# Kernel optimization log

Measured on AMD Instinct MI355X. Metric: run time of the kernel, lower is better.

The kernel has to match this reference:

```python
import jax, jax.numpy as jnp
import numpy as np
import math

B, N, D, H = 2, 2048, 512, 8
DH = D // H
HID = int(D * 16 / 3)  # 2730, SwiGLU hidden; chunks into 1365+1365
EPS = 1e-5


def _get_slopes(n):
    # n=8 is a power of two
    start = 2.0 ** (-2.0 ** (-(math.log2(n) - 3)))
    return np.array([start * (start ** i) for i in range(n)], dtype=np.float32)

_SLOPES = jnp.asarray(_get_slopes(H))  # [H]


def _ln(x, w, b):
    m = jnp.mean(x, axis=-1, keepdims=True)
    v = jnp.mean((x - m) ** 2, axis=-1, keepdims=True)
    return (x - m) * jax.lax.rsqrt(v + EPS) * w + b


def setup_inputs() -> dict:
    key = jax.random.key(0)
    ks = jax.random.split(key, 20)
    p = lambda k, s: jax.random.normal(k, s, jnp.float32) * 0.02
    return {
        "x": jax.random.normal(ks[0], (B, N, D), jnp.float32),
        "coords": jax.random.uniform(ks[1], (B, N, 2), jnp.float32) * 100.0,
        "q_w": p(ks[2], (D, D)), "q_b": jnp.zeros((D,), jnp.float32),
        "k_w": p(ks[3], (D, D)), "k_b": jnp.zeros((D,), jnp.float32),
        "v_w": p(ks[4], (D, D)), "v_b": jnp.zeros((D,), jnp.float32),
        "o_w": p(ks[5], (D, D)), "o_b": jnp.zeros((D,), jnp.float32),
        "gamma1": jnp.ones((D,), jnp.float32),
        "ln1_w": jnp.ones((D,), jnp.float32), "ln1_b": jnp.zeros((D,), jnp.float32),
        "fc1_w": p(ks[6], (HID, D)), "fc1_b": jnp.zeros((HID,), jnp.float32),
        "fc2_w": p(ks[7], (D, HID // 2)), "fc2_b": jnp.zeros((D,), jnp.float32),
        "gamma2": jnp.ones((D,), jnp.float32),
        "ln2_w": jnp.ones((D,), jnp.float32), "ln2_b": jnp.zeros((D,), jnp.float32),
    }


def reference(x, coords, q_w, q_b, k_w, k_b, v_w, v_b, o_w, o_b, gamma1,
              ln1_w, ln1_b, fc1_w, fc1_b, fc2_w, fc2_b, gamma2, ln2_w, ln2_b):
    # ---- residual1: distance-ALiBi attention (eval mode: x + gamma1*attn(norm(x)))
    xn = _ln(x, ln1_w, ln1_b)
    q = (xn @ q_w.T + q_b).reshape(B, N, H, DH).transpose(0, 2, 1, 3)  # [b,h,n,dh]
    k = (xn @ k_w.T + k_b).reshape(B, N, H, DH).transpose(0, 2, 1, 3)
    v = (xn @ v_w.T + v_b).reshape(B, N, H, DH).transpose(0, 2, 1, 3)
    # pairwise Euclidean distance of tile coords -> [b,n,n]
    diff = coords[:, :, None, :] - coords[:, None, :, :]
    dist = jnp.sqrt(jnp.sum(diff * diff, axis=-1))
    attn_bias = -_SLOPES[None, :, None, None] * dist[:, None, :, :]  # [b,h,n,n]
    scale = 1.0 / math.sqrt(DH)
    scores = jnp.einsum('bhqd,bhkd->bhqk', q, k) * scale + attn_bias
    attn = jax.nn.softmax(scores, axis=-1)
    ctx = jnp.einsum('bhqk,bhkd->bhqd', attn, v)
    ctx = ctx.transpose(0, 2, 1, 3).reshape(B, N, D)
    attn_out = ctx @ o_w.T + o_b
    x = x + gamma1 * attn_out
    # ---- residual2: SwiGLU-style MLP (eval mode: x + gamma2*mlp(norm(x)))
    xn2 = _ln(x, ln2_w, ln2_b)
    hpre = xn2 @ fc1_w.T + fc1_b  # [b,n,HID]
    h1, h2 = jnp.split(hpre, 2, axis=-1)
    mlp_out = (jax.nn.silu(h1) * h2) @ fc2_w.T + fc2_b
    return x + gamma2 * mlp_out
```

## Files before the change

kernel.cpp:

```cpp
#include <hip/hip_runtime.h>
#include <math.h>

#define Bdim  2
#define Nseq  2048
#define Dmod  512
#define Hn    8
#define DHd   64
#define HID   2730
#define HHALF 1365
#define HC    1408
#define NPACK 2816
#define ROWS  4096
#define NSPLIT 2

typedef __bf16 bf16x8 __attribute__((ext_vector_type(8)));
typedef __bf16 bf16x4 __attribute__((ext_vector_type(4)));
typedef __bf16 bf16x2 __attribute__((ext_vector_type(2)));
typedef float  f32x4  __attribute__((ext_vector_type(4)));

__device__ __forceinline__ void glds16(const __bf16* g, __bf16* l) {
    __builtin_amdgcn_global_load_lds(
        (const __attribute__((address_space(1))) void*)g,
        (__attribute__((address_space(3))) void*)l, 16, 0, 0);
}

__device__ __forceinline__ void ln_core(
    int tid, float vx, float vy, const float* __restrict__ w,
    const float* __restrict__ b, __bf16* __restrict__ orow)
{
    float s  = vx + vy;
    float sq = vx * vx + vy * vy;
#pragma unroll
    for (int m = 1; m < 64; m <<= 1) {
        s  += __shfl_xor(s, m, 64);
        sq += __shfl_xor(sq, m, 64);
    }
    __shared__ float ss[4], ssq[4];
    const int wv = tid >> 6;
    if ((tid & 63) == 0) { ss[wv] = s; ssq[wv] = sq; }
    __syncthreads();
    s  = ss[0] + ss[1] + ss[2] + ss[3];
    sq = ssq[0] + ssq[1] + ssq[2] + ssq[3];
    const float mean = s * (1.0f / Dmod);
    const float var  = sq * (1.0f / Dmod) - mean * mean;
    const float rstd = rsqrtf(var + 1e-5f);
    float2 wv2 = *(const float2*)(w + tid * 2);
    float2 bv2 = *(const float2*)(b + tid * 2);
    orow[0] = (__bf16)((vx - mean) * rstd * wv2.x + bv2.x);
    orow[1] = (__bf16)((vy - mean) * rstd * wv2.y + bv2.y);
}

#define SEG0 (1536*512)
#define SEG1 (512*512)
#define SEG2 (NPACK*512)
#define SEG3 (512*HC)
#define CONV_BLOCKS ((SEG0 + SEG1 + SEG2 + SEG3) / 256)
__global__ __launch_bounds__(256) void convert_ln(
    const float* __restrict__ q_w, const float* __restrict__ k_w,
    const float* __restrict__ v_w, const float* __restrict__ o_w,
    const float* __restrict__ fc1_w, const float* __restrict__ fc2_w,
    __bf16* __restrict__ wqkv, __bf16* __restrict__ wo,
    __bf16* __restrict__ wfc1p, __bf16* __restrict__ wfc2p,
    const float* __restrict__ x, const float* __restrict__ ln1w,
    const float* __restrict__ ln1b, __bf16* __restrict__ xn)
{
    if (blockIdx.x >= CONV_BLOCKS) {
        const int row = blockIdx.x - CONV_BLOCKS, tid = threadIdx.x;
        float2 v = *(const float2*)(x + (size_t)row * Dmod + tid * 2);
        ln_core(tid, v.x, v.y, ln1w, ln1b, xn + (size_t)row * Dmod + tid * 2);
        return;
    }
    int idx = blockIdx.x * 256 + threadIdx.x;
    if (idx < SEG0) {
        int n = idx >> 9, k = idx & 511;
        float v = (n < 512) ? q_w[n * 512 + k]
                : (n < 1024) ? k_w[(n - 512) * 512 + k]
                : v_w[(n - 1024) * 512 + k];
        wqkv[idx] = (__bf16)v;
        return;
    }
    idx -= SEG0;
    if (idx < SEG1) { wo[idx] = (__bf16)o_w[idx]; return; }
    idx -= SEG1;
    if (idx < SEG2) {
        int n = idx >> 9, k = idx & 511;
        int j = n >> 5, u = n & 31;
        int base = j * 16 + (u & 15);
        float v = 0.0f;
        if (base < HHALF) {
            int hidx = base + ((u & 16) ? HHALF : 0);
            v = fc1_w[(size_t)hidx * 512 + k];
        }
        wfc1p[idx] = (__bf16)v;
        return;
    }
    idx -= SEG2;
    if (idx < SEG3) {
        int n = idx / HC, k = idx - n * HC;
        float v = (k < HHALF) ? fc2_w[(size_t)n * HHALF + k] : 0.0f;
        wfc2p[idx] = (__bf16)v;
    }
}

__global__ __launch_bounds__(256) void ln_kernel_bf16(
    const __bf16* __restrict__ x, const float* __restrict__ w,
    const float* __restrict__ b, __bf16* __restrict__ out)
{
    const int row = blockIdx.x, tid = threadIdx.x;
    bf16x2 v2 = *(const bf16x2*)(x + (size_t)row * Dmod + tid * 2);
    ln_core(tid, (float)v2[0], (float)v2[1], w, b, out + (size_t)row * Dmod + tid * 2);
}

template<int MODE>
__global__ __launch_bounds__(512) void gemm_res(
    const __bf16* __restrict__ A, int lda,
    const __bf16* __restrict__ opA, const float* __restrict__ lpA,
    const __bf16* __restrict__ Bw, int ldb,
    const float* __restrict__ bias, int K,
    void* __restrict__ outp, const void* __restrict__ resp,
    const float* __restrict__ g)
{
    __shared__ __bf16 smem[2 * 64 * 64];
    __bf16* As = smem;
    __bf16* Bs = smem + 64 * 64;
    const int tid  = threadIdx.x;
    const int wave = tid >> 6, lane = tid & 63;
    const int t    = lane & 15, quad = lane >> 4;
    const int kg   = wave >> 2, wv = wave & 3;
    const int m0   = blockIdx.x * 64;
    const int n0   = blockIdx.y * 64;

    const int srow = tid >> 3;
    const int gch  = ((tid & 7) ^ (srow & 7)) * 8;
    const int grow = m0 + srow;
    const int bI   = grow >> 11, nn = grow & 2047;
    const __bf16* aptr = A  + (size_t)grow * lda + gch;
    const __bf16* bptr = Bw + (size_t)(n0 + srow) * ldb + gch;

    const int arow = wv * 16 + t;
    const int aoff = arow * 64 + (((kg * 4 + quad) ^ (arow & 7)) * 8);
    int boffs[4];
#pragma unroll
    for (int ct = 0; ct < 4; ++ct) {
        int brow = ct * 16 + t;
        boffs[ct] = brow * 64 + (((kg * 4 + quad) ^ (brow & 7)) * 8);
    }

    f32x4 acc[4] = {};
    for (int k0 = 0; k0 < K; k0 += 64) {
        __syncthreads();
        if (MODE == 0) {
            const int kk = k0 + gch;
            const int h = kk >> 6;
            float l = lpA[((size_t)(bI * Hn) + h) * Nseq + nn]
                    + lpA[((size_t)((Bdim + bI) * Hn) + h) * Nseq + nn];
            float rl = __builtin_amdgcn_rcpf(l);
            bf16x8 a0 = *(const bf16x8*)(opA + (size_t)grow * Dmod + kk);
            bf16x8 a1 = *(const bf16x8*)(opA + ((size_t)ROWS + grow) * Dmod + kk);
            bf16x8 mg;
#pragma unroll
            for (int j = 0; j < 8; ++j)
                mg[j] = (__bf16)(((float)a0[j] + (float)a1[j]) * rl);
            *(bf16x8*)(As + tid * 8) = mg;
        } else {
            glds16(aptr + k0, As + tid * 8);
        }
        glds16(bptr + k0, Bs + tid * 8);
        __syncthreads();
        bf16x8 a = *(const bf16x8*)(As + aoff);
#pragma unroll
        for (int ct = 0; ct < 4; ++ct) {
            bf16x8 b = *(const bf16x8*)(Bs + boffs[ct]);
            acc[ct] = __builtin_amdgcn_mfma_f32_16x16x32_bf16(a, b, acc[ct], 0, 0, 0);
        }
    }

    __syncthreads();
    if (kg == 1) {
        float* dst = (float*)smem + ((size_t)wv * 64 + lane) * 16;
#pragma unroll
        for (int ct = 0; ct < 4; ++ct) *(f32x4*)(dst + ct * 4) = acc[ct];
    }
    __syncthreads();
    if (kg == 0) {
        const float* src = (const float*)smem + ((size_t)wv * 64 + lane) * 16;
        const int row_base = m0 + wv * 16 + quad * 4;
#pragma unroll
        for (int ct = 0; ct < 4; ++ct) {
            f32x4 other = *(const f32x4*)(src + ct * 4);
            const int col = n0 + ct * 16 + t;
            const float bb = bias[col];
#pragma unroll
            for (int r = 0; r < 4; ++r) {
                const int row = row_base + r;
                const float v = (acc[ct][r] + other[r] + bb) * g[col];
                if (MODE == 0) {
                    float rv = ((const float*)resp)[(size_t)row * Dmod + col];
                    ((__bf16*)outp)[(size_t)row * Dmod + col] = (__bf16)(rv + v);
                } else {
                    float rv = (float)((const __bf16*)resp)[(size_t)row * Dmod + col];
                    ((float*)outp)[(size_t)row * Dmod + col] = rv + v;
                }
            }
        }
    }
}

#define LDT 136
__global__ __launch_bounds__(256) void qkv_gemm128(
    const __bf16* __restrict__ A, const __bf16* __restrict__ W,
    const float* __restrict__ qb_, const float* __restrict__ kb_,
    const float* __restrict__ vb_,
    __bf16* __restrict__ qk, __bf16* __restrict__ vtg)
{
    __shared__ __bf16 smem[64 * LDT];
    __bf16* As = smem;
    __bf16* Bs = smem + 4096;
    const int tid  = threadIdx.x;
    const int wave = tid >> 6, lane = tid & 63;
    const int t    = lane & 15, quad = lane >> 4;
    const int m0   = blockIdx.x * 128, n0 = blockIdx.y * 128;
    const int mr   = (wave & 1) * 64,  nr = (wave >> 1) * 64;
    const int ra0 = tid >> 2,          ca0 = (tid & 3) * 8;
    const int ra1 = (tid + 256) >> 2,  ca1 = (tid & 3) * 8;

    f32x4 acc[4][4] = {};

    for (int k0 = 0; k0 < Dmod; k0 += 32) {
        __syncthreads();
        glds16(A + (size_t)(m0 + ra0) * Dmod + k0 + ca0, As + tid * 8);
        glds16(A + (size_t)(m0 + ra1) * Dmod + k0 + ca1, As + (tid + 256) * 8);
        glds16(W + (size_t)(n0 + ra0) * Dmod + k0 + ca0, Bs + tid * 8);
        glds16(W + (size_t)(n0 + ra1) * Dmod + k0 + ca1, Bs + (tid + 256) * 8);
        __syncthreads();
        bf16x8 af[4], bfr[4];
#pragma unroll
        for (int mi = 0; mi < 4; ++mi)
            af[mi] = *(const bf16x8*)(As + (mr + mi * 16 + t) * 32 + quad * 8);
#pragma unroll
        for (int ni = 0; ni < 4; ++ni)
            bfr[ni] = *(const bf16x8*)(Bs + (nr + ni * 16 + t) * 32 + quad * 8);
#pragma unroll
        for (int mi = 0; mi < 4; ++mi)
#pragma unroll
            for (int ni = 0; ni < 4; ++ni)
                acc[mi][ni] = __builtin_amdgcn_mfma_f32_16x16x32_bf16(af[mi], bfr[ni], acc[mi][ni], 0, 0, 0);
    }

    const int y = blockIdx.y;
    if (y < 8) {
#pragma unroll
        for (int mi = 0; mi < 4; ++mi) {
            const int row_base = m0 + mr + mi * 16 + quad * 4;
#pragma unroll
            for (int ni = 0; ni < 4; ++ni) {
                const int col = n0 + nr + ni * 16 + t;
                const float bb = (col < 512) ? qb_[col] : kb_[col - 512];
#pragma unroll
                for (int r = 0; r < 4; ++r)
                    qk[(size_t)(row_base + r) * 1024 + col] = (__bf16)(acc[mi][ni][r] + bb);
            }
        }
    } else {
        const int tok0 = m0 & 2047;
        const int bI   = m0 >> 11;
#pragma unroll
        for (int half = 0; half < 2; ++half) {
            __syncthreads();
            if ((wave >> 1) == half) {
#pragma unroll
                for (int ni = 0; ni < 4; ++ni) {
                    const int dh = ni * 16 + t;
                    const float bb = vb_[(y - 8) * 128 + half * 64 + dh];
#pragma unroll
                    for (int mi = 0; mi < 4; ++mi) {
                        const int n = mr + mi * 16 + quad * 4;
                        bf16x4 pk;
#pragma unroll
                        for (int r = 0; r < 4; ++r) pk[r] = (__bf16)(acc[mi][ni][r] + bb);
                        *(bf16x4*)(smem + dh * LDT + n) = pk;
                    }
                }
            }
            __syncthreads();
            const int hh = (y - 8) * 2 + half;
            const size_t rowbase = (size_t)(bI * 8 + hh) * 64;
#pragma unroll
            for (int j = 0; j < 4; ++j) {
                int chunk = tid + j * 256;
                int dr = chunk >> 4, cc = (chunk & 15) * 8;
                bf16x8 vv = *(const bf16x8*)(smem + dr * LDT + cc);
                *(bf16x8*)(vtg + (rowbase + dr) * Nseq + tok0 + cc) = vv;
            }
        }
    }
}

__global__ __launch_bounds__(256) void fc1_gemm128(
    const __bf16* __restrict__ A, const __bf16* __restrict__ W,
    const float* __restrict__ fc1_b_, __bf16* __restrict__ out)
{
    __shared__ __bf16 As[128 * 32];
    __shared__ __bf16 Bs[128 * 32];
    const int tid  = threadIdx.x;
    const int wave = tid >> 6, lane = tid & 63;
    const int t    = lane & 15, quad = lane >> 4;
    const int m0   = blockIdx.x * 128, n0 = blockIdx.y * 128;
    const int mr   = (wave & 1) * 64,  nr = (wave >> 1) * 64;
    const int ra0 = tid >> 2,          ca0 = (tid & 3) * 8;
    const int ra1 = (tid + 256) >> 2,  ca1 = (tid & 3) * 8;

    f32x4 acc[4][4] = {};

    for (int k0 = 0; k0 < Dmod; k0 += 32) {
        __syncthreads();
        glds16(A + (size_t)(m0 + ra0) * Dmod + k0 + ca0, As + tid * 8);
        glds16(A + (size_t)(m0 + ra1) * Dmod + k0 + ca1, As + (tid + 256) * 8);
        glds16(W + (size_t)(n0 + ra0) * Dmod + k0 + ca0, Bs + tid * 8);
        glds16(W + (size_t)(n0 + ra1) * Dmod + k0 + ca1, Bs + (tid + 256) * 8);
        __syncthreads();
        bf16x8 af[4], bfr[4];
#pragma unroll
        for (int mi = 0; mi < 4; ++mi)
            af[mi] = *(const bf16x8*)(As + (mr + mi * 16 + t) * 32 + quad * 8);
#pragma unroll
        for (int ni = 0; ni < 4; ++ni)
            bfr[ni] = *(const bf16x8*)(Bs + (nr + ni * 16 + t) * 32 + quad * 8);
#pragma unroll
        for (int mi = 0; mi < 4; ++mi)
#pragma unroll
            for (int ni = 0; ni < 4; ++ni)
                acc[mi][ni] = __builtin_amdgcn_mfma_f32_16x16x32_bf16(af[mi], bfr[ni], acc[mi][ni], 0, 0, 0);
    }

#pragma unroll
    for (int mi = 0; mi < 4; ++mi) {
        const int row_base = m0 + mr + mi * 16 + quad * 4;
#pragma unroll
        for (int gI = 0; gI < 2; ++gI) {
            const int base = n0 + nr + gI * 32;
            const int hb = (base >> 5) * 16 + t;
            const bool valid = hb < HHALF;
            const float b1 = valid ? fc1_b_[hb] : 0.0f;
            const float b2 = valid ? fc1_b_[HHALF + hb] : 0.0f;
#pragma unroll
            for (int r = 0; r < 4; ++r) {
                float a = acc[mi][2 * gI][r] + b1;
                float c = acc[mi][2 * gI + 1][r] + b2;
                float sw = a / (1.0f + __expf(-a)) * c;
                out[(size_t)(row_base + r) * HC + hb] = (__bf16)sw;
            }
        }
    }
}

__global__ __launch_bounds__(256) void attn_kernel(
    const __bf16* __restrict__ qk, const __bf16* __restrict__ vt,
    const float* __restrict__ coords,
    __bf16* __restrict__ op, float* __restrict__ lp, int ktper)
{
    constexpr int LD = 72;
    __shared__ __bf16 Ks[64][LD];
    __shared__ __bf16 Vt[64][LD];
    __shared__ __bf16 Ps[64][LD];
    __shared__ float2 kco[64];

    const int qt = blockIdx.x, h = blockIdx.y;
    const int s = blockIdx.z >> 1, b = blockIdx.z & 1;
    const int bh = b * Hn + h;
    const int tid = threadIdx.x;
    const int wave = tid >> 6, lane = tid & 63;
    const int t = lane & 15, quad = lane >> 4;
    const float c1 = 0.125f * 1.44269504f;
    const float d1 = exp2f(-(float)(h + 1)) * 1.44269504f;

    const int qrow = qt * 64 + wave * 16 + t;
    const size_t qbase = (size_t)(b * Nseq + qrow) * 1024 + h * DHd;
    bf16x8 bq0 = *(const bf16x8*)(qk + qbase + quad * 8);
    bf16x8 bq1 = *(const bf16x8*)(qk + qbase + 32 + quad * 8);
    float2 qc = *(const float2*)(coords + (size_t)(b * Nseq + qrow) * 2);
    const float qx = qc.x, qy = qc.y;

    const int sr = tid >> 3, scc = (tid & 7) * 8;
    const __bf16* kbase = qk + (size_t)(b * Nseq) * 1024 + 512 + h * DHd;
    const __bf16* vbase = vt + (size_t)(bh * 64) * Nseq;

    bf16x8 kreg0, kreg1, vreg0, vreg1;
    float2 kcreg = {0.f, 0.f};
    int kn = s * ktper * 64;
    kreg0 = *(const bf16x8*)(kbase + (size_t)(kn + sr) * 1024 + scc);
    kreg1 = *(const bf16x8*)(kbase + (size_t)(kn + sr + 32) * 1024 + scc);
    vreg0 = *(const bf16x8*)(vbase + (size_t)sr * Nseq + kn + scc);
    vreg1 = *(const bf16x8*)(vbase + (size_t)(sr + 32) * Nseq + kn + scc);
    if (tid < 64) kcreg = *(const float2*)(coords + (size_t)(b * Nseq + kn + tid) * 2);

    f32x4 o[4] = {};
    float lrun = 0.0f;

    for (int it = 0; it < ktper; ++it) {
        __syncthreads();
        *(bf16x8*)(&Ks[sr][scc])      = kreg0;
        *(bf16x8*)(&Ks[sr + 32][scc]) = kreg1;
        *(bf16x8*)(&Vt[sr][scc])      = vreg0;
        *(bf16x8*)(&Vt[sr + 32][scc]) = vreg1;
        if (tid < 64) kco[tid] = kcreg;
        __syncthreads();
        if (it + 1 < ktper) {
            const int k2 = kn + 64;
            kreg0 = *(const bf16x8*)(kbase + (size_t)(k2 + sr) * 1024 + scc);
            kreg1 = *(const bf16x8*)(kbase + (size_t)(k2 + sr + 32) * 1024 + scc);
            vreg0 = *(const bf16x8*)(vbase + (size_t)sr * Nseq + k2 + scc);
            vreg1 = *(const bf16x8*)(vbase + (size_t)(sr + 32) * Nseq + k2 + scc);
            if (tid < 64) kcreg = *(const float2*)(coords + (size_t)(b * Nseq + k2 + tid) * 2);
        }

        f32x4 sA[4];
#pragma unroll
        for (int am = 0; am < 4; ++am) {
            bf16x8 a0 = *(const bf16x8*)(&Ks[am * 16 + t][quad * 8]);
            bf16x8 a1 = *(const bf16x8*)(&Ks[am * 16 + t][32 + quad * 8]);
            f32x4 z = {};
            z = __builtin_amdgcn_mfma_f32_16x16x32_bf16(a0, bq0, z, 0, 0, 0);
            sA[am] = __builtin_amdgcn_mfma_f32_16x16x32_bf16(a1, bq1, z, 0, 0, 0);
        }

        float p[4][4];
#pragma unroll
        for (int am = 0; am < 4; ++am)
#pragma unroll
            for (int r = 0; r < 4; ++r) {
                float2 kc = kco[am * 16 + quad * 4 + r];
                float dx = qx - kc.x, dy = qy - kc.y;
                float dist = __builtin_amdgcn_sqrtf(dx * dx + dy * dy);
                float e = __builtin_amdgcn_exp2f(sA[am][r] * c1 - d1 * dist);
                p[am][r] = e;
                lrun += e;
            }

#pragma unroll
        for (int am = 0; am < 4; ++am) {
            bf16x4 pk;
#pragma unroll
            for (int r = 0; r < 4; ++r) pk[r] = (__bf16)p[am][r];
            *(bf16x4*)(&Ps[wave * 16 + t][am * 16 + quad * 4]) = pk;
        }

        bf16x8 ap0 = *(const bf16x8*)(&Ps[wave * 16 + t][quad * 8]);
        bf16x8 ap1 = *(const bf16x8*)(&Ps[wave * 16 + t][32 + quad * 8]);
#pragma unroll
        for (int ct = 0; ct < 4; ++ct) {
            bf16x8 bv0 = *(const bf16x8*)(&Vt[ct * 16 + t][quad * 8]);
            bf16x8 bv1 = *(const bf16x8*)(&Vt[ct * 16 + t][32 + quad * 8]);
            o[ct] = __builtin_amdgcn_mfma_f32_16x16x32_bf16(ap0, bv0, o[ct], 0, 0, 0);
            o[ct] = __builtin_amdgcn_mfma_f32_16x16x32_bf16(ap1, bv1, o[ct], 0, 0, 0);
        }
        kn += 64;
    }

    lrun += __shfl_xor(lrun, 16, 64);
    lrun += __shfl_xor(lrun, 32, 64);
    if (quad == 0)
        lp[(((size_t)s * Bdim + b) * Hn + h) * Nseq + qt * 64 + wave * 16 + t] = lrun;

    const int orow_base = qt * 64 + wave * 16 + quad * 4;
#pragma unroll
    for (int ct = 0; ct < 4; ++ct)
#pragma unroll
        for (int r = 0; r < 4; ++r) {
            size_t row = (size_t)s * ROWS + b * Nseq + orow_base + r;
            op[row * Dmod + h * DHd + ct * 16 + t] = (__bf16)o[ct][r];
        }
}

extern "C" void kernel_launch(void* const* d_in, const int* in_sizes, int n_in,
                              void* d_out, int out_size, void* d_ws, size_t ws_size,
                              hipStream_t stream)
{
    (void)in_sizes; (void)n_in; (void)out_size; (void)ws_size;
    const float* x      = (const float*)d_in[0];
    const float* coords = (const float*)d_in[1];
    const float* q_w    = (const float*)d_in[2];
    const float* q_b    = (const float*)d_in[3];
    const float* k_w    = (const float*)d_in[4];
    const float* k_b    = (const float*)d_in[5];
    const float* v_w    = (const float*)d_in[6];
    const float* v_b    = (const float*)d_in[7];
    const float* o_w    = (const float*)d_in[8];
    const float* o_b    = (const float*)d_in[9];
    const float* gamma1 = (const float*)d_in[10];
    const float* ln1_w  = (const float*)d_in[11];
    const float* ln1_b  = (const float*)d_in[12];
    const float* fc1_w  = (const float*)d_in[13];
    const float* fc1_b  = (const float*)d_in[14];
    const float* fc2_w  = (const float*)d_in[15];
    const float* fc2_b  = (const float*)d_in[16];
    const float* gamma2 = (const float*)d_in[17];
    const float* ln2_w  = (const float*)d_in[18];
    const float* ln2_b  = (const float*)d_in[19];

    size_t off = 0;
    auto alloc = [&](size_t bytes) {
        void* p = (char*)d_ws + off;
        off += (bytes + 255) & ~(size_t)255;
        return p;
    };
    __bf16* wqkv  = (__bf16*)alloc((size_t)1536 * 512 * 2);
    __bf16* wo    = (__bf16*)alloc((size_t)512 * 512 * 2);
    __bf16* wfc1p = (__bf16*)alloc((size_t)NPACK * 512 * 2);
    __bf16* wfc2p = (__bf16*)alloc((size_t)512 * HC * 2);
    __bf16* xn    = (__bf16*)alloc((size_t)ROWS * Dmod * 2);
    __bf16* xn2   = (__bf16*)alloc((size_t)ROWS * Dmod * 2);
    __bf16* qkb   = (__bf16*)alloc((size_t)ROWS * 1024 * 2);
    __bf16* vtg   = (__bf16*)alloc((size_t)Bdim * Hn * DHd * Nseq * 2);
    __bf16* x1    = (__bf16*)alloc((size_t)ROWS * Dmod * 2);
    __bf16* hcomb = (__bf16*)alloc((size_t)ROWS * HC * 2);
    __bf16* opb   = (__bf16*)alloc((size_t)NSPLIT * ROWS * Dmod * 2);
    float*  lpb   = (float*)alloc((size_t)NSPLIT * Bdim * Hn * Nseq * 4);

    convert_ln<<<CONV_BLOCKS + ROWS, 256, 0, stream>>>(
        q_w, k_w, v_w, o_w, fc1_w, fc2_w, wqkv, wo, wfc1p, wfc2p,
        x, ln1_w, ln1_b, xn);

    qkv_gemm128<<<dim3(ROWS / 128, 12), 256, 0, stream>>>(xn, wqkv, q_b, k_b, v_b, qkb, vtg);

    attn_kernel<<<dim3(Nseq / 64, Hn, Bdim * NSPLIT), 256, 0, stream>>>(
        qkb, vtg, coords, opb, lpb, Nseq / 64 / NSPLIT);

    gemm_res<0><<<dim3(ROWS / 64, Dmod / 64), 512, 0, stream>>>(
        nullptr, Dmod, opb, lpb, wo, Dmod, o_b, Dmod, (void*)x1, (const void*)x, gamma1);

    ln_kernel_bf16<<<ROWS, 256, 0, stream>>>(x1, ln2_w, ln2_b, xn2);

    fc1_gemm128<<<dim3(ROWS / 128, NPACK / 128), 256, 0, stream>>>(xn2, wfc1p, fc1_b, hcomb);

    gemm_res<1><<<dim3(ROWS / 64, Dmod / 64), 512, 0, stream>>>(
        hcomb, HC, nullptr, nullptr, wfc2p, HC, fc2_b, HC, d_out, (const void*)x1, gamma2);
}
```

Baseline: 213.5 us.

## Fuse LN2 into o-proj epilogue and fc1 prologue; overlap weight conversion with attention

The o-projection epilogue now accumulates per-row sum and sum-of-squares with atomics. The fc1 GEMM applies layernorm on the fly from those statistics when it loads A tiles, so the separate LN2 kernel and the xn2 buffer go away. Conversion of the o, fc1 and fc2 weights moves out of the first kernel and into extra blocks of the attention launch, so it runs alongside attention rather than ahead of it. In exchange, fc1 loses the async global-to-LDS load for A and recomputes normalization in every N-tile block, and the atomics plus the one-pass variance add some cost and numerical risk.

```diff
diff --git a/kernel.cpp b/kernel.cpp
--- a/kernel.cpp
+++ b/kernel.cpp
@@ -15,7 +15,6 @@
 
 typedef __bf16 bf16x8 __attribute__((ext_vector_type(8)));
 typedef __bf16 bf16x4 __attribute__((ext_vector_type(4)));
-typedef __bf16 bf16x2 __attribute__((ext_vector_type(2)));
 typedef float  f32x4  __attribute__((ext_vector_type(4)));
 
 __device__ __forceinline__ void glds16(const __bf16* g, __bf16* l) {
@@ -23,6 +22,15 @@
         (const __attribute__((address_space(1))) void*)g,
         (__attribute__((address_space(3))) void*)l, 16, 0, 0);
 }
+
+#define SEG0 (1536*512)
+#define SEG1 (512*512)
+#define SEG2 (NPACK*512)
+#define SEG3 (512*HC)
+#define WQKV_BLOCKS (SEG0 / 256)
+#define ZERO_BLOCKS 32
+#define REST_BLOCKS ((SEG1 + SEG2 + SEG3) / 256)
+#define REST_Z (REST_BLOCKS / (32 * 8))
 
 __device__ __forceinline__ void ln_core(
     int tid, float vx, float vy, const float* __restrict__ w,
@@ -50,28 +58,15 @@
     orow[1] = (__bf16)((vy - mean) * rstd * wv2.y + bv2.y);
 }
 
-#define SEG0 (1536*512)
-#define SEG1 (512*512)
-#define SEG2 (NPACK*512)
-#define SEG3 (512*HC)
-#define CONV_BLOCKS ((SEG0 + SEG1 + SEG2 + SEG3) / 256)
-__global__ __launch_bounds__(256) void convert_ln(
+__global__ __launch_bounds__(256) void prep_kernel(
     const float* __restrict__ q_w, const float* __restrict__ k_w,
-    const float* __restrict__ v_w, const float* __restrict__ o_w,
-    const float* __restrict__ fc1_w, const float* __restrict__ fc2_w,
-    __bf16* __restrict__ wqkv, __bf16* __restrict__ wo,
-    __bf16* __restrict__ wfc1p, __bf16* __restrict__ wfc2p,
+    const float* __restrict__ v_w, __bf16* __restrict__ wqkv,
     const float* __restrict__ x, const float* __restrict__ ln1w,
-    const float* __restrict__ ln1b, __bf16* __restrict__ xn)
-{
-    if (blockIdx.x >= CONV_BLOCKS) {
-        const int row = blockIdx.x - CONV_BLOCKS, tid = threadIdx.x;
-        float2 v = *(const float2*)(x + (size_t)row * Dmod + tid * 2);
-        ln_core(tid, v.x, v.y, ln1w, ln1b, xn + (size_t)row * Dmod + tid * 2);
-        return;
-    }
-    int idx = blockIdx.x * 256 + threadIdx.x;
-    if (idx < SEG0) {
+    const float* __restrict__ ln1b, __bf16* __restrict__ xn,
+    float* __restrict__ rstats)
+{
+    if (blockIdx.x < WQKV_BLOCKS) {
+        int idx = blockIdx.x * 256 + threadIdx.x;
         int n = idx >> 9, k = idx & 511;
         float v = (n < 512) ? q_w[n * 512 + k]
                 : (n < 1024) ? k_w[(n - 512) * 512 + k]
@@ -79,36 +74,13 @@
         wqkv[idx] = (__bf16)v;
         return;
     }
-    idx -= SEG0;
-    if (idx < SEG1) { wo[idx] = (__bf16)o_w[idx]; return; }
-    idx -= SEG1;
-    if (idx < SEG2) {
-        int n = idx >> 9, k = idx & 511;
-        int j = n >> 5, u = n & 31;
-        int base = j * 16 + (u & 15);
-        float v = 0.0f;
-        if (base < HHALF) {
-            int hidx = base + ((u & 16) ? HHALF : 0);
-            v = fc1_w[(size_t)hidx * 512 + k];
-        }
-        wfc1p[idx] = (__bf16)v;
+    if (blockIdx.x < WQKV_BLOCKS + ZERO_BLOCKS) {
+        rstats[(blockIdx.x - WQKV_BLOCKS) * 256 + threadIdx.x] = 0.0f;
         return;
     }
-    idx -= SEG2;
-    if (idx < SEG3) {
-        int n = idx / HC, k = idx - n * HC;
-        float v = (k < HHALF) ? fc2_w[(size_t)n * HHALF + k] : 0.0f;
-        wfc2p[idx] = (__bf16)v;
-    }
-}
-
-__global__ __launch_bounds__(256) void ln_kernel_bf16(
-    const __bf16* __restrict__ x, const float* __restrict__ w,
-    const float* __restrict__ b, __bf16* __restrict__ out)
-{
-    const int row = blockIdx.x, tid = threadIdx.x;
-    bf16x2 v2 = *(const bf16x2*)(x + (size_t)row * Dmod + tid * 2);
-    ln_core(tid, (float)v2[0], (float)v2[1], w, b, out + (size_t)row * Dmod + tid * 2);
+    const int row = blockIdx.x - WQKV_BLOCKS - ZERO_BLOCKS, tid = threadIdx.x;
+    float2 v = *(const float2*)(x + (size_t)row * Dmod + tid * 2);
+    ln_core(tid, v.x, v.y, ln1w, ln1b, xn + (size_t)row * Dmod + tid * 2);
 }
 
 template<int MODE>
@@ -118,7 +90,7 @@
     const __bf16* __restrict__ Bw, int ldb,
     const float* __restrict__ bias, int K,
     void* __restrict__ outp, const void* __restrict__ resp,
-    const float* __restrict__ g)
+    const float* __restrict__ g, float* __restrict__ rstats)
 {
     __shared__ __bf16 smem[2 * 64 * 64];
     __bf16* As = smem;
@@ -185,6 +157,8 @@
     if (kg == 0) {
         const float* src = (const float*)smem + ((size_t)wv * 64 + lane) * 16;
         const int row_base = m0 + wv * 16 + quad * 4;
+        float rsum[4] = {0.f, 0.f, 0.f, 0.f};
+        float rsq[4]  = {0.f, 0.f, 0.f, 0.f};
 #pragma unroll
         for (int ct = 0; ct < 4; ++ct) {
             f32x4 other = *(const f32x4*)(src + ct * 4);
@@ -196,10 +170,31 @@
                 const float v = (acc[ct][r] + other[r] + bb) * g[col];
                 if (MODE == 0) {
                     float rv = ((const float*)resp)[(size_t)row * Dmod + col];
-                    ((__bf16*)outp)[(size_t)row * Dmod + col] = (__bf16)(rv + v);
+                    __bf16 xv = (__bf16)(rv + v);
+                    ((__bf16*)outp)[(size_t)row * Dmod + col] = xv;
+                    float xf = (float)xv;
+                    rsum[r] += xf;
+                    rsq[r]  += xf * xf;
                 } else {
                     float rv = (float)((const __bf16*)resp)[(size_t)row * Dmod + col];
                     ((float*)outp)[(size_t)row * Dmod + col] = rv + v;
+                }
+            }
+        }
+        if (MODE == 0) {
+#pragma unroll
+            for (int r = 0; r < 4; ++r) {
+#pragma unroll
+                for (int msk = 1; msk < 16; msk <<= 1) {
+                    rsum[r] += __shfl_xor(rsum[r], msk, 64);
+                    rsq[r]  += __shfl_xor(rsq[r],  msk, 64);
+                }
+            }
+            if (t == 0) {
+#pragma unroll
+                for (int r = 0; r < 4; ++r) {
+                    atomicAdd(&rstats[(size_t)(row_base + r) * 2],     rsum[r]);
+                    atomicAdd(&rstats[(size_t)(row_base + r) * 2 + 1], rsq[r]);
                 }
             }
         }
@@ -297,7 +292,9 @@
 }
 
 __global__ __launch_bounds__(256) void fc1_gemm128(
-    const __bf16* __restrict__ A, const __bf16* __restrict__ W,
+    const __bf16* __restrict__ x1, const float* __restrict__ rstats,
+    const float* __restrict__ ln2w, const float* __restrict__ ln2b,
+    const __bf16* __restrict__ W,
     const float* __restrict__ fc1_b_, __bf16* __restrict__ out)
 {
     __shared__ __bf16 As[128 * 32];
@@ -310,12 +307,34 @@
     const int ra0 = tid >> 2,          ca0 = (tid & 3) * 8;
     const int ra1 = (tid + 256) >> 2,  ca1 = (tid & 3) * 8;
 
+    const int gr0 = m0 + ra0, gr1 = m0 + ra1;
+    const float s0  = rstats[(size_t)gr0 * 2],     q0 = rstats[(size_t)gr0 * 2 + 1];
+    const float s1  = rstats[(size_t)gr1 * 2],     q1 = rstats[(size_t)gr1 * 2 + 1];
+    const float mean0 = s0 * (1.0f / Dmod);
+    const float mean1 = s1 * (1.0f / Dmod);
+    const float rstd0 = rsqrtf(q0 * (1.0f / Dmod) - mean0 * mean0 + 1e-5f);
+    const float rstd1 = rsqrtf(q1 * (1.0f / Dmod) - mean1 * mean1 + 1e-5f);
+
     f32x4 acc[4][4] = {};
 
     for (int k0 = 0; k0 < Dmod; k0 += 32) {
         __syncthreads();
-        glds16(A + (size_t)(m0 + ra0) * Dmod + k0 + ca0, As + tid * 8);
-        glds16(A + (size_t)(m0 + ra1) * Dmod + k0 + ca1, As + (tid + 256) * 8);
+        float4 w0 = *(const float4*)(ln2w + k0 + ca0);
+        float4 w1 = *(const float4*)(ln2w + k0 + ca0 + 4);
+        float4 b0 = *(const float4*)(ln2b + k0 + ca0);
+        float4 b1 = *(const float4*)(ln2b + k0 + ca0 + 4);
+        float ws[8] = {w0.x, w0.y, w0.z, w0.w, w1.x, w1.y, w1.z, w1.w};
+        float bs[8] = {b0.x, b0.y, b0.z, b0.w, b1.x, b1.y, b1.z, b1.w};
+        bf16x8 v0 = *(const bf16x8*)(x1 + (size_t)gr0 * Dmod + k0 + ca0);
+        bf16x8 v1 = *(const bf16x8*)(x1 + (size_t)gr1 * Dmod + k0 + ca1);
+        bf16x8 n0v, n1v;
+#pragma unroll
+        for (int j = 0; j < 8; ++j) {
+            n0v[j] = (__bf16)(((float)v0[j] - mean0) * rstd0 * ws[j] + bs[j]);
+            n1v[j] = (__bf16)(((float)v1[j] - mean1) * rstd1 * ws[j] + bs[j]);
+        }
+        *(bf16x8*)(As + tid * 8)         = n0v;
+        *(bf16x8*)(As + (tid + 256) * 8) = n1v;
         glds16(W + (size_t)(n0 + ra0) * Dmod + k0 + ca0, Bs + tid * 8);
         glds16(W + (size_t)(n0 + ra1) * Dmod + k0 + ca1, Bs + (tid + 256) * 8);
         __syncthreads();
@@ -357,13 +376,41 @@
 __global__ __launch_bounds__(256) void attn_kernel(
     const __bf16* __restrict__ qk, const __bf16* __restrict__ vt,
     const float* __restrict__ coords,
-    __bf16* __restrict__ op, float* __restrict__ lp, int ktper)
+    __bf16* __restrict__ op, float* __restrict__ lp, int ktper,
+    const float* __restrict__ o_w, const float* __restrict__ fc1_w,
+    const float* __restrict__ fc2_w,
+    __bf16* __restrict__ wo, __bf16* __restrict__ wfc1p,
+    __bf16* __restrict__ wfc2p)
 {
     constexpr int LD = 72;
     __shared__ __bf16 Ks[64][LD];
     __shared__ __bf16 Vt[64][LD];
     __shared__ __bf16 Ps[64][LD];
     __shared__ float2 kco[64];
+
+    if (blockIdx.z >= Bdim * NSPLIT) {
+        int cidx = ((blockIdx.z - Bdim * NSPLIT) * 8 + blockIdx.y) * 32 + blockIdx.x;
+        int idx = cidx * 256 + threadIdx.x;
+        if (idx < SEG1) { wo[idx] = (__bf16)o_w[idx]; return; }
+        idx -= SEG1;
+        if (idx < SEG2) {
+            int n = idx >> 9, k = idx & 511;
+            int j = n >> 5, u = n & 31;
+            int base = j * 16 + (u & 15);
+            float v = 0.0f;
+            if (base < HHALF) {
+                int hidx = base + ((u & 16) ? HHALF : 0);
+                v = fc1_w[(size_t)hidx * 512 + k];
+            }
+            wfc1p[idx] = (__bf16)v;
+            return;
+        }
+        idx -= SEG2;
+        int n = idx / HC, k = idx - n * HC;
+        float v = (k < HHALF) ? fc2_w[(size_t)n * HHALF + k] : 0.0f;
+        wfc2p[idx] = (__bf16)v;
+        return;
+    }
 
     const int qt = blockIdx.x, h = blockIdx.y;
     const int s = blockIdx.z >> 1, b = blockIdx.z & 1;
@@ -509,30 +556,31 @@
     __bf16* wfc1p = (__bf16*)alloc((size_t)NPACK * 512 * 2);
     __bf16* wfc2p = (__bf16*)alloc((size_t)512 * HC * 2);
     __bf16* xn    = (__bf16*)alloc((size_t)ROWS * Dmod * 2);
-    __bf16* xn2   = (__bf16*)alloc((size_t)ROWS * Dmod * 2);
     __bf16* qkb   = (__bf16*)alloc((size_t)ROWS * 1024 * 2);
     __bf16* vtg   = (__bf16*)alloc((size_t)Bdim * Hn * DHd * Nseq * 2);
     __bf16* x1    = (__bf16*)alloc((size_t)ROWS * Dmod * 2);
     __bf16* hcomb = (__bf16*)alloc((size_t)ROWS * HC * 2);
     __bf16* opb   = (__bf16*)alloc((size_t)NSPLIT * ROWS * Dmod * 2);
     float*  lpb   = (float*)alloc((size_t)NSPLIT * Bdim * Hn * Nseq * 4);
-
-    convert_ln<<<CONV_BLOCKS + ROWS, 256, 0, stream>>>(
-        q_w, k_w, v_w, o_w, fc1_w, fc2_w, wqkv, wo, wfc1p, wfc2p,
-        x, ln1_w, ln1_b, xn);
+    float*  rstats = (float*)alloc((size_t)ROWS * 2 * 4);
+
+    prep_kernel<<<WQKV_BLOCKS + ZERO_BLOCKS + ROWS, 256, 0, stream>>>(
+        q_w, k_w, v_w, wqkv, x, ln1_w, ln1_b, xn, rstats);
 
     qkv_gemm128<<<dim3(ROWS / 128, 12), 256, 0, stream>>>(xn, wqkv, q_b, k_b, v_b, qkb, vtg);
 
-    attn_kernel<<<dim3(Nseq / 64, Hn, Bdim * NSPLIT), 256, 0, stream>>>(
-        qkb, vtg, coords, opb, lpb, Nseq / 64 / NSPLIT);
+    attn_kernel<<<dim3(Nseq / 64, Hn, Bdim * NSPLIT + REST_Z), 256, 0, stream>>>(
+        qkb, vtg, coords, opb, lpb, Nseq / 64 / NSPLIT,
+        o_w, fc1_w, fc2_w, wo, wfc1p, wfc2p);
 
     gemm_res<0><<<dim3(ROWS / 64, Dmod / 64), 512, 0, stream>>>(
-        nullptr, Dmod, opb, lpb, wo, Dmod, o_b, Dmod, (void*)x1, (const void*)x, gamma1);
-
-    ln_kernel_bf16<<<ROWS, 256, 0, stream>>>(x1, ln2_w, ln2_b, xn2);
-
-    fc1_gemm128<<<dim3(ROWS / 128, NPACK / 128), 256, 0, stream>>>(xn2, wfc1p, fc1_b, hcomb);
+        nullptr, Dmod, opb, lpb, wo, Dmod, o_b, Dmod, (void*)x1, (const void*)x,
+        gamma1, rstats);
+
+    fc1_gemm128<<<dim3(ROWS / 128, NPACK / 128), 256, 0, stream>>>(
+        x1, rstats, ln2_w, ln2_b, wfc1p, fc1_b, hcomb);
 
     gemm_res<1><<<dim3(ROWS / 64, Dmod / 64), 512, 0, stream>>>(
-        hcomb, HC, nullptr, nullptr, wfc2p, HC, fc2_b, HC, d_out, (const void*)x1, gamma2);
-}
+        hcomb, HC, nullptr, nullptr, wfc2p, HC, fc2_b, HC, d_out, (const void*)x1,
+        gamma2, nullptr);
+}
```

Result: slower. 219.0 us (+2.6%).

## Move o/fc1/fc2 weight conversion into extra attention-kernel blocks to fill tail

Applied to the files above, without the earlier changes.

Only the QKV weight conversion and LN1 stay in the first kernel, which is renamed prep_kernel. The o_w, fc1_w and fc2_w fp32-to-bf16 conversions and packing move into extra z-slices of the attention launch. Those blocks return before any attention work. The goal is to take that conversion off the critical path before the QKV GEMM and let it fill idle CUs during the attention kernel's tail. In exchange, the extra blocks reserve the attention kernel's static shared memory and add a branch to every attention block.

```diff
diff --git a/kernel.cpp b/kernel.cpp
--- a/kernel.cpp
+++ b/kernel.cpp
@@ -23,6 +23,14 @@
         (const __attribute__((address_space(1))) void*)g,
         (__attribute__((address_space(3))) void*)l, 16, 0, 0);
 }
+
+#define SEG0 (1536*512)
+#define SEG1 (512*512)
+#define SEG2 (NPACK*512)
+#define SEG3 (512*HC)
+#define WQKV_BLOCKS (SEG0 / 256)
+#define REST_BLOCKS ((SEG1 + SEG2 + SEG3) / 256)
+#define REST_Z (REST_BLOCKS / (32 * 8))
 
 __device__ __forceinline__ void ln_core(
     int tid, float vx, float vy, const float* __restrict__ w,
@@ -50,28 +58,14 @@
     orow[1] = (__bf16)((vy - mean) * rstd * wv2.y + bv2.y);
 }
 
-#define SEG0 (1536*512)
-#define SEG1 (512*512)
-#define SEG2 (NPACK*512)
-#define SEG3 (512*HC)
-#define CONV_BLOCKS ((SEG0 + SEG1 + SEG2 + SEG3) / 256)
-__global__ __launch_bounds__(256) void convert_ln(
+__global__ __launch_bounds__(256) void prep_kernel(
     const float* __restrict__ q_w, const float* __restrict__ k_w,
-    const float* __restrict__ v_w, const float* __restrict__ o_w,
-    const float* __restrict__ fc1_w, const float* __restrict__ fc2_w,
-    __bf16* __restrict__ wqkv, __bf16* __restrict__ wo,
-    __bf16* __restrict__ wfc1p, __bf16* __restrict__ wfc2p,
+    const float* __restrict__ v_w, __bf16* __restrict__ wqkv,
     const float* __restrict__ x, const float* __restrict__ ln1w,
     const float* __restrict__ ln1b, __bf16* __restrict__ xn)
 {
-    if (blockIdx.x >= CONV_BLOCKS) {
-        const int row = blockIdx.x - CONV_BLOCKS, tid = threadIdx.x;
-        float2 v = *(const float2*)(x + (size_t)row * Dmod + tid * 2);
-        ln_core(tid, v.x, v.y, ln1w, ln1b, xn + (size_t)row * Dmod + tid * 2);
-        return;
-    }
-    int idx = blockIdx.x * 256 + threadIdx.x;
-    if (idx < SEG0) {
+    if (blockIdx.x < WQKV_BLOCKS) {
+        int idx = blockIdx.x * 256 + threadIdx.x;
         int n = idx >> 9, k = idx & 511;
         float v = (n < 512) ? q_w[n * 512 + k]
                 : (n < 1024) ? k_w[(n - 512) * 512 + k]
@@ -79,27 +73,9 @@
         wqkv[idx] = (__bf16)v;
         return;
     }
-    idx -= SEG0;
-    if (idx < SEG1) { wo[idx] = (__bf16)o_w[idx]; return; }
-    idx -= SEG1;
-    if (idx < SEG2) {
-        int n = idx >> 9, k = idx & 511;
-        int j = n >> 5, u = n & 31;
-        int base = j * 16 + (u & 15);
-        float v = 0.0f;
-        if (base < HHALF) {
-            int hidx = base + ((u & 16) ? HHALF : 0);
-            v = fc1_w[(size_t)hidx * 512 + k];
-        }
-        wfc1p[idx] = (__bf16)v;
-        return;
-    }
-    idx -= SEG2;
-    if (idx < SEG3) {
-        int n = idx / HC, k = idx - n * HC;
-        float v = (k < HHALF) ? fc2_w[(size_t)n * HHALF + k] : 0.0f;
-        wfc2p[idx] = (__bf16)v;
-    }
+    const int row = blockIdx.x - WQKV_BLOCKS, tid = threadIdx.x;
+    float2 v = *(const float2*)(x + (size_t)row * Dmod + tid * 2);
+    ln_core(tid, v.x, v.y, ln1w, ln1b, xn + (size_t)row * Dmod + tid * 2);
 }
 
 __global__ __launch_bounds__(256) void ln_kernel_bf16(
@@ -357,13 +333,41 @@
 __global__ __launch_bounds__(256) void attn_kernel(
     const __bf16* __restrict__ qk, const __bf16* __restrict__ vt,
     const float* __restrict__ coords,
-    __bf16* __restrict__ op, float* __restrict__ lp, int ktper)
+    __bf16* __restrict__ op, float* __restrict__ lp, int ktper,
+    const float* __restrict__ o_w, const float* __restrict__ fc1_w,
+    const float* __restrict__ fc2_w,
+    __bf16* __restrict__ wo, __bf16* __restrict__ wfc1p,
+    __bf16* __restrict__ wfc2p)
 {
     constexpr int LD = 72;
     __shared__ __bf16 Ks[64][LD];
     __shared__ __bf16 Vt[64][LD];
     __shared__ __bf16 Ps[64][LD];
     __shared__ float2 kco[64];
+
+    if (blockIdx.z >= Bdim * NSPLIT) {
+        int cidx = ((blockIdx.z - Bdim * NSPLIT) * 8 + blockIdx.y) * 32 + blockIdx.x;
+        int idx = cidx * 256 + threadIdx.x;
+        if (idx < SEG1) { wo[idx] = (__bf16)o_w[idx]; return; }
+        idx -= SEG1;
+        if (idx < SEG2) {
+            int n = idx >> 9, k = idx & 511;
+            int j = n >> 5, u = n & 31;
+            int base = j * 16 + (u & 15);
+            float v = 0.0f;
+            if (base < HHALF) {
+                int hidx = base + ((u & 16) ? HHALF : 0);
+                v = fc1_w[(size_t)hidx * 512 + k];
+            }
+            wfc1p[idx] = (__bf16)v;
+            return;
+        }
+        idx -= SEG2;
+        int n = idx / HC, k = idx - n * HC;
+        float v = (k < HHALF) ? fc2_w[(size_t)n * HHALF + k] : 0.0f;
+        wfc2p[idx] = (__bf16)v;
+        return;
+    }
 
     const int qt = blockIdx.x, h = blockIdx.y;
     const int s = blockIdx.z >> 1, b = blockIdx.z & 1;
@@ -517,14 +521,14 @@
     __bf16* opb   = (__bf16*)alloc((size_t)NSPLIT * ROWS * Dmod * 2);
     float*  lpb   = (float*)alloc((size_t)NSPLIT * Bdim * Hn * Nseq * 4);
 
-    convert_ln<<<CONV_BLOCKS + ROWS, 256, 0, stream>>>(
-        q_w, k_w, v_w, o_w, fc1_w, fc2_w, wqkv, wo, wfc1p, wfc2p,
-        x, ln1_w, ln1_b, xn);
+    prep_kernel<<<WQKV_BLOCKS + ROWS, 256, 0, stream>>>(
+        q_w, k_w, v_w, wqkv, x, ln1_w, ln1_b, xn);
 
     qkv_gemm128<<<dim3(ROWS / 128, 12), 256, 0, stream>>>(xn, wqkv, q_b, k_b, v_b, qkb, vtg);
 
-    attn_kernel<<<dim3(Nseq / 64, Hn, Bdim * NSPLIT), 256, 0, stream>>>(
-        qkb, vtg, coords, opb, lpb, Nseq / 64 / NSPLIT);
+    attn_kernel<<<dim3(Nseq / 64, Hn, Bdim * NSPLIT + REST_Z), 256, 0, stream>>>(
+        qkb, vtg, coords, opb, lpb, Nseq / 64 / NSPLIT,
+        o_w, fc1_w, fc2_w, wo, wfc1p, wfc2p);
 
     gemm_res<0><<<dim3(ROWS / 64, Dmod / 64), 512, 0, stream>>>(
         nullptr, Dmod, opb, lpb, wo, Dmod, o_b, Dmod, (void*)x1, (const void*)x, gamma1);
```

Result: no change. 211.0 us (-1.2%).
